# Performance work log

Hardware: AMD Instinct MI355X
Metric: run time of the kernel (lower is better)

Reference implementation:

```python
import jax, jax.numpy as jnp
import numpy as np

EPS = 1e-8  # torch cosine_similarity default eps


def setup_inputs() -> dict:
    key = jax.random.key(0)
    k1, k2, k3 = jax.random.split(key, 3)
    bsz, sent_len, cont_dim, mp_dim = 16, 512, 768, 20
    repres = jax.random.normal(k1, (bsz, sent_len, cont_dim), dtype=jnp.float32)
    max_att = jax.random.normal(k2, (bsz, sent_len, cont_dim), dtype=jnp.float32)
    # nn.Parameter initialized uniform_(-1, 1)
    weight = jax.random.uniform(k3, (mp_dim, cont_dim), dtype=jnp.float32, minval=-1.0, maxval=1.0)
    return {"repres": repres, "max_att": max_att, "weight": weight}


def reference(repres, max_att, weight):
    # Original math: a = repres[:,None,:] * w[None], b = max_att[:,None,:] * w[None]
    # cos = <a,b> / (max(||a||,eps) * max(||b||,eps)) along last dim.
    # Fused form: never materialize [N, mp_dim, cont_dim]; contract with w^2 directly.
    bsz, sent_len, cont_dim = repres.shape
    r = repres.reshape(-1, cont_dim)   # [N, D]
    m = max_att.reshape(-1, cont_dim)  # [N, D]
    w2 = weight * weight               # [P, D]
    dot = jnp.einsum('nd,pd->np', r * m, w2)              # [N, P]
    n1 = jnp.sqrt(jnp.einsum('nd,pd->np', r * r, w2))     # [N, P]
    n2 = jnp.sqrt(jnp.einsum('nd,pd->np', m * m, w2))     # [N, P]
    cos = dot / (jnp.maximum(n1, EPS) * jnp.maximum(n2, EPS))
    return cos.reshape(bsz, sent_len, weight.shape[0])
```

## Files before the change

kernel.cpp:

```cpp
#include <hip/hip_runtime.h>
#include <math.h>
#include <stdint.h>

static constexpr int D_DIM   = 768;
static constexpr int NP      = 20;
static constexpr int NROWS   = 8192;
static constexpr int ROWS_PB = 16;
static constexpr int BLOCKS  = NROWS / ROWS_PB;
static constexpr int KW      = 192;
static constexpr int KSLICE  = 32;
static constexpr int NSLICES = KW / KSLICE;

typedef short  short8  __attribute__((ext_vector_type(8)));
typedef float  float4v __attribute__((ext_vector_type(4)));

static constexpr int A_WAVE = 8192;
static constexpr int A_BUF  = 4096;
static constexpr int A_MAT  = 2048;
static constexpr int B_OFF  = 32768;
static constexpr int B_CSTR = 776 * 2;
static constexpr int LDS_SZ = B_OFF + NP * B_CSTR;

__device__ __forceinline__ void async_copy16(const void* g, void* l) {
  __builtin_amdgcn_global_load_lds(
      (const __attribute__((address_space(1))) unsigned int*)(uintptr_t)g,
      (__attribute__((address_space(3))) unsigned int*)(uint32_t)(uintptr_t)l,
      16, 0, 0);
}

__device__ __forceinline__ unsigned short bf16_rne(float x) {
  unsigned u = __float_as_uint(x);
  u += 0x7FFFu + ((u >> 16) & 1u);
  return (unsigned short)(u >> 16);
}
__device__ __forceinline__ float bf16f(unsigned short h) {
  return __uint_as_float(((unsigned)h) << 16);
}

__global__ __launch_bounds__(256) void atte_cos_mfma(
    const float* __restrict__ repres,
    const float* __restrict__ max_att,
    const float* __restrict__ weight,
    float* __restrict__ out)
{
  const int tid  = threadIdx.x;
  const int wave = tid >> 6;
  const int lane = tid & 63;
  const int row0 = blockIdx.x * ROWS_PB;
  const int k0   = wave * KW;
  const int part = lane >> 4;
  const int mrow = lane & 15;

  __shared__ __align__(16) char smem[LDS_SZ];
  char* a_base = smem + wave * A_WAVE;

  auto stage = [&](int s, int b) {
#pragma unroll
    for (int j = 0; j < 2; ++j) {
      const int slot = j * 64 + lane;
      const int row  = slot >> 3;
      const int gp   = slot & 7;
      const int gl   = (gp - 2 * (row & 3)) & 7;
      const float* gr = repres  + (size_t)(row0 + row) * D_DIM + k0 + s * KSLICE + gl * 4;
      const float* gm = max_att + (size_t)(row0 + row) * D_DIM + k0 + s * KSLICE + gl * 4;
      char* la = a_base + b * A_BUF + slot * 16;
      async_copy16(gr, la);
      async_copy16(gm, la + A_MAT);
    }
  };

  stage(0, 0);
  stage(1, 1);

  for (int col = 0; col < NP; ++col) {
#pragma unroll
    for (int j = 0; j < 3; ++j) {
      const int k = j * 256 + tid;
      const float wv = weight[col * D_DIM + k];
      *(unsigned short*)(smem + B_OFF + col * B_CSTR + k * 2) = bf16_rne(wv * wv);
    }
  }

  __syncthreads();

  const int a_off = mrow * 128 + (((part + (mrow & 3)) & 3) * 32);
  const char* b0p = smem + B_OFF + (lane & 15) * B_CSTR + (k0 + part * 8) * 2;
  const int c1col = min(16 + (lane & 15), NP - 1);
  const char* b1p = smem + B_OFF + c1col * B_CSTR + (k0 + part * 8) * 2;

  float4v acc[6] = {};

#pragma unroll
  for (int s = 0; s < NSLICES; ++s) {
    __builtin_amdgcn_s_waitcnt(0x0F74);
    const char* ab = a_base + (s & 1) * A_BUF;

    float rv[8], mv[8];
    *(float4*)&rv[0] = *(const float4*)(ab + a_off);
    *(float4*)&rv[4] = *(const float4*)(ab + a_off + 16);
    *(float4*)&mv[0] = *(const float4*)(ab + A_MAT + a_off);
    *(float4*)&mv[4] = *(const float4*)(ab + A_MAT + a_off + 16);

    short8 a0h, a0l, a1h, a2h;
#pragma unroll
    for (int j = 0; j < 8; ++j) {
      const float pm = rv[j] * mv[j];
      const float pr = rv[j] * rv[j];
      const float pq = mv[j] * mv[j];
      const unsigned short h = bf16_rne(pm);
      a0h[j] = (short)h;
      a0l[j] = (short)bf16_rne(pm - bf16f(h));
      a1h[j] = (short)bf16_rne(pr);
      a2h[j] = (short)bf16_rne(pq);
    }

    const short8 b0 = *(const short8*)(b0p + s * 64);
    const short8 b1 = *(const short8*)(b1p + s * 64);

    acc[0] = __builtin_amdgcn_mfma_f32_16x16x32_bf16(a0h, b0, acc[0], 0, 0, 0);
    acc[0] = __builtin_amdgcn_mfma_f32_16x16x32_bf16(a0l, b0, acc[0], 0, 0, 0);
    acc[1] = __builtin_amdgcn_mfma_f32_16x16x32_bf16(a0h, b1, acc[1], 0, 0, 0);
    acc[1] = __builtin_amdgcn_mfma_f32_16x16x32_bf16(a0l, b1, acc[1], 0, 0, 0);
    acc[2] = __builtin_amdgcn_mfma_f32_16x16x32_bf16(a1h, b0, acc[2], 0, 0, 0);
    acc[3] = __builtin_amdgcn_mfma_f32_16x16x32_bf16(a1h, b1, acc[3], 0, 0, 0);
    acc[4] = __builtin_amdgcn_mfma_f32_16x16x32_bf16(a2h, b0, acc[4], 0, 0, 0);
    acc[5] = __builtin_amdgcn_mfma_f32_16x16x32_bf16(a2h, b1, acc[5], 0, 0, 0);

    if (s + 2 < NSLICES) {
      __builtin_amdgcn_s_waitcnt(0xC07F);
      stage(s + 2, s & 1);
    }
  }

  __syncthreads();
#pragma unroll
  for (int qc = 0; qc < 6; ++qc)
    *(float4v*)(smem + ((qc * 4 + wave) * 64 + lane) * 16) = acc[qc];
  __syncthreads();

  if (wave < 2) {
    const int ct = wave;
    float4v c0 = {}, c1 = {}, c2 = {};
#pragma unroll
    for (int wv = 0; wv < 4; ++wv) {
      c0 += *(const float4v*)(smem + (((0 * 2 + ct) * 4 + wv) * 64 + lane) * 16);
      c1 += *(const float4v*)(smem + (((1 * 2 + ct) * 4 + wv) * 64 + lane) * 16);
      c2 += *(const float4v*)(smem + (((2 * 2 + ct) * 4 + wv) * 64 + lane) * 16);
    }
    const int col = ct * 16 + (lane & 15);
    if (col < NP) {
      const int rbase = row0 + (lane >> 4) * 4;
#pragma unroll
      for (int r = 0; r < 4; ++r) {
        const float n1 = fmaxf(sqrtf(c1[r]), 1e-8f);
        const float n2 = fmaxf(sqrtf(c2[r]), 1e-8f);
        out[(size_t)(rbase + r) * NP + col] = c0[r] / (n1 * n2);
      }
    }
  }
}

extern "C" void kernel_launch(void* const* d_in, const int* in_sizes, int n_in,
                              void* d_out, int out_size, void* d_ws, size_t ws_size,
                              hipStream_t stream) {
  const float* repres  = (const float*)d_in[0];
  const float* max_att = (const float*)d_in[1];
  const float* weight  = (const float*)d_in[2];
  float* out = (float*)d_out;

  atte_cos_mfma<<<BLOCKS, 256, 0, stream>>>(repres, max_att, weight, out);
}
```

Baseline: 88.19 us.

## Load activations straight into registers and vectorize weight-square staging

Activation slices are no longer staged through LDS with async global-to-LDS copies. Each lane now loads its own 8-float chunks of repres and max_att directly into registers, double-buffered two slices ahead. This removes the A staging region, so shared memory per block roughly halves, which can let more blocks share a CU. The squared-weight bf16 table is also built with float4 loads and 4-wide stores instead of scalar ones. The catch is that per-lane global loads are less coalesced across rows and the register prefetch uses more VGPRs.

```diff
diff --git a/kernel.cpp b/kernel.cpp
--- a/kernel.cpp
+++ b/kernel.cpp
@@ -1,12 +1,14 @@
 #include <hip/hip_runtime.h>
 #include <math.h>
 #include <stdint.h>
+
 
 static constexpr int D_DIM   = 768;
 static constexpr int NP      = 20;
 static constexpr int NROWS   = 8192;
 static constexpr int ROWS_PB = 16;
 static constexpr int BLOCKS  = NROWS / ROWS_PB;
+static constexpr int NTHR    = 256;
 static constexpr int KW      = 192;
 static constexpr int KSLICE  = 32;
 static constexpr int NSLICES = KW / KSLICE;
@@ -14,19 +16,8 @@
 typedef short  short8  __attribute__((ext_vector_type(8)));
 typedef float  float4v __attribute__((ext_vector_type(4)));
 
-static constexpr int A_WAVE = 8192;
-static constexpr int A_BUF  = 4096;
-static constexpr int A_MAT  = 2048;
-static constexpr int B_OFF  = 32768;
 static constexpr int B_CSTR = 776 * 2;
-static constexpr int LDS_SZ = B_OFF + NP * B_CSTR;
-
-__device__ __forceinline__ void async_copy16(const void* g, void* l) {
-  __builtin_amdgcn_global_load_lds(
-      (const __attribute__((address_space(1))) unsigned int*)(uintptr_t)g,
-      (__attribute__((address_space(3))) unsigned int*)(uint32_t)(uintptr_t)l,
-      16, 0, 0);
-}
+static constexpr int LDS_SZ = NP * B_CSTR;
 
 __device__ __forceinline__ unsigned short bf16_rne(float x) {
   unsigned u = __float_as_uint(x);
@@ -37,7 +28,7 @@
   return __uint_as_float(((unsigned)h) << 16);
 }
 
-__global__ __launch_bounds__(256) void atte_cos_mfma(
+__global__ __launch_bounds__(NTHR) void atte_cos_v3(
     const float* __restrict__ repres,
     const float* __restrict__ max_att,
     const float* __restrict__ weight,
@@ -51,55 +42,60 @@
   const int part = lane >> 4;
   const int mrow = lane & 15;
 
-  __shared__ __align__(16) char smem[LDS_SZ];
-  char* a_base = smem + wave * A_WAVE;
+  __shared__ __align__(16) char smem[31104];
 
-  auto stage = [&](int s, int b) {
+  const float* ar = repres  + (size_t)(row0 + mrow) * D_DIM + k0 + part * 8;
+  const float* am = max_att + (size_t)(row0 + mrow) * D_DIM + k0 + part * 8;
+
+  float4 fr[2][2], fm[2][2];
+  fr[0][0] = *(const float4*)(ar + 0 * KSLICE);
+  fr[0][1] = *(const float4*)(ar + 0 * KSLICE + 4);
+  fm[0][0] = *(const float4*)(am + 0 * KSLICE);
+  fm[0][1] = *(const float4*)(am + 0 * KSLICE + 4);
+  fr[1][0] = *(const float4*)(ar + 1 * KSLICE);
+  fr[1][1] = *(const float4*)(ar + 1 * KSLICE + 4);
+  fm[1][0] = *(const float4*)(am + 1 * KSLICE);
+  fm[1][1] = *(const float4*)(am + 1 * KSLICE + 4);
+
+  {
+    const float4* wsrc = (const float4*)weight;
 #pragma unroll
-    for (int j = 0; j < 2; ++j) {
-      const int slot = j * 64 + lane;
-      const int row  = slot >> 3;
-      const int gp   = slot & 7;
-      const int gl   = (gp - 2 * (row & 3)) & 7;
-      const float* gr = repres  + (size_t)(row0 + row) * D_DIM + k0 + s * KSLICE + gl * 4;
-      const float* gm = max_att + (size_t)(row0 + row) * D_DIM + k0 + s * KSLICE + gl * 4;
-      char* la = a_base + b * A_BUF + slot * 16;
-      async_copy16(gr, la);
-      async_copy16(gm, la + A_MAT);
-    }
-  };
-
-  stage(0, 0);
-  stage(1, 1);
-
-  for (int col = 0; col < NP; ++col) {
-#pragma unroll
-    for (int j = 0; j < 3; ++j) {
-      const int k = j * 256 + tid;
-      const float wv = weight[col * D_DIM + k];
-      *(unsigned short*)(smem + B_OFF + col * B_CSTR + k * 2) = bf16_rne(wv * wv);
+    for (int it = 0; it < 15; ++it) {
+      const int i   = it * NTHR + tid;
+      const int col = i / 192;
+      const int kq  = i - col * 192;
+      float4 w = wsrc[i];
+      ushort4 h;
+      h.x = bf16_rne(w.x * w.x);
+      h.y = bf16_rne(w.y * w.y);
+      h.z = bf16_rne(w.z * w.z);
+      h.w = bf16_rne(w.w * w.w);
+      *(ushort4*)(smem + col * B_CSTR + kq * 8) = h;
     }
   }
 
   __syncthreads();
 
-  const int a_off = mrow * 128 + (((part + (mrow & 3)) & 3) * 32);
-  const char* b0p = smem + B_OFF + (lane & 15) * B_CSTR + (k0 + part * 8) * 2;
-  const int c1col = min(16 + (lane & 15), NP - 1);
-  const char* b1p = smem + B_OFF + c1col * B_CSTR + (k0 + part * 8) * 2;
+  const char* b0p = smem + (lane & 15) * B_CSTR + (k0 + part * 8) * 2;
+  const int   c1c = min(16 + (lane & 15), NP - 1);
+  const char* b1p = smem + c1c * B_CSTR + (k0 + part * 8) * 2;
 
   float4v acc[6] = {};
 
 #pragma unroll
   for (int s = 0; s < NSLICES; ++s) {
-    __builtin_amdgcn_s_waitcnt(0x0F74);
-    const char* ab = a_base + (s & 1) * A_BUF;
+    float rv[8], mv[8];
+    *(float4*)&rv[0] = fr[s & 1][0];
+    *(float4*)&rv[4] = fr[s & 1][1];
+    *(float4*)&mv[0] = fm[s & 1][0];
+    *(float4*)&mv[4] = fm[s & 1][1];
 
-    float rv[8], mv[8];
-    *(float4*)&rv[0] = *(const float4*)(ab + a_off);
-    *(float4*)&rv[4] = *(const float4*)(ab + a_off + 16);
-    *(float4*)&mv[0] = *(const float4*)(ab + A_MAT + a_off);
-    *(float4*)&mv[4] = *(const float4*)(ab + A_MAT + a_off + 16);
+    if (s + 2 < NSLICES) {
+      fr[s & 1][0] = *(const float4*)(ar + (s + 2) * KSLICE);
+      fr[s & 1][1] = *(const float4*)(ar + (s + 2) * KSLICE + 4);
+      fm[s & 1][0] = *(const float4*)(am + (s + 2) * KSLICE);
+      fm[s & 1][1] = *(const float4*)(am + (s + 2) * KSLICE + 4);
+    }
 
     short8 a0h, a0l, a1h, a2h;
 #pragma unroll
@@ -125,11 +121,6 @@
     acc[3] = __builtin_amdgcn_mfma_f32_16x16x32_bf16(a1h, b1, acc[3], 0, 0, 0);
     acc[4] = __builtin_amdgcn_mfma_f32_16x16x32_bf16(a2h, b0, acc[4], 0, 0, 0);
     acc[5] = __builtin_amdgcn_mfma_f32_16x16x32_bf16(a2h, b1, acc[5], 0, 0, 0);
-
-    if (s + 2 < NSLICES) {
-      __builtin_amdgcn_s_waitcnt(0xC07F);
-      stage(s + 2, s & 1);
-    }
   }
 
   __syncthreads();
@@ -163,10 +154,7 @@
 extern "C" void kernel_launch(void* const* d_in, const int* in_sizes, int n_in,
                               void* d_out, int out_size, void* d_ws, size_t ws_size,
                               hipStream_t stream) {
-  const float* repres  = (const float*)d_in[0];
-  const float* max_att = (const float*)d_in[1];
-  const float* weight  = (const float*)d_in[2];
-  float* out = (float*)d_out;
-
-  atte_cos_mfma<<<BLOCKS, 256, 0, stream>>>(repres, max_att, weight, out);
+  atte_cos_v3<<<BLOCKS, NTHR, 0, stream>>>(
+      (const float*)d_in[0], (const float*)d_in[1],
+      (const float*)d_in[2], (float*)d_out);
 }
```

New measurement: 90.72 us. 1.03x slower.
